# Kernel optimization log

Measured on AMD Instinct MI355X. Metric: run time of the kernel, lower is better.

## Reference

```python
import jax, jax.numpy as jnp
import numpy as np

B, N, D_MODEL = 2, 2048, 1024
H, HEAD_DIM, D1 = 16, 128, 2048
NK, RANK = 16, 32
GAMMA = 0.999


def setup_inputs() -> dict:
    key = jax.random.key(0)
    ks = jax.random.split(key, 12)
    std = 0.02
    return {
        "x": jax.random.normal(ks[0], (B, N, D_MODEL), jnp.float32),
        "Wu": jax.random.normal(ks[1], (D_MODEL, D1), jnp.float32) * std,
        "bu": jax.random.normal(ks[2], (D1,), jnp.float32) * std,
        "Wv": jax.random.normal(ks[3], (D_MODEL, D1), jnp.float32) * std,
        "bv": jax.random.normal(ks[4], (D1,), jnp.float32) * std,
        "Wo": jax.random.normal(ks[5], (D1, D_MODEL), jnp.float32) * std,
        "bo": jax.random.normal(ks[6], (D_MODEL,), jnp.float32) * std,
        # SKI low-rank Toeplitz kernel factors at nk inducing relative positions
        "a_pos": jax.random.normal(ks[7], (H, NK, RANK), jnp.float32) * 0.1,
        "b_pos": jax.random.normal(ks[8], (H, RANK, HEAD_DIM), jnp.float32) * 0.1,
        "a_neg": jax.random.normal(ks[9], (H, NK, RANK), jnp.float32) * 0.1,
        "b_neg": jax.random.normal(ks[10], (H, RANK, HEAD_DIM), jnp.float32) * 0.1,
        "t_zero": jax.random.normal(ks[11], (H, HEAD_DIM), jnp.float32) * 0.1,
    }


def _interp_decay_kernel(a, b, n):
    # low-rank kernel at nk inducing points: [h, nk, d]
    k_ind = jnp.einsum("hkr,hrd->hkd", a, b)
    lags = jnp.arange(1, n)                      # lags 1..n-1
    p = (lags - 1.0) / (n - 2.0) * (NK - 1)      # map lag onto inducing grid
    lo = jnp.floor(p).astype(jnp.int32)
    hi = jnp.minimum(lo + 1, NK - 1)
    w = (p - lo)[None, :, None]
    k = k_ind[:, lo, :] * (1.0 - w) + k_ind[:, hi, :] * w  # [h, n-1, d]
    decay = (GAMMA ** lags)[None, :, None]
    return k * decay


def reference(x, Wu, bu, Wv, bv, Wo, bo, a_pos, b_pos, a_neg, b_neg, t_zero):
    u = jax.nn.silu(x @ Wu + bu)                 # [b, n, d1]
    v = jax.nn.silu(x @ Wv + bv)                 # [b, n, d1]
    n = v.shape[1]
    vh = v.reshape(v.shape[0], n, H, HEAD_DIM)   # [b, n, h, d]

    kp = _interp_decay_kernel(a_pos, b_pos, n)   # [h, n-1, d]
    kn = _interp_decay_kernel(a_neg, b_neg, n)   # [h, n-1, d]
    m = 2 * n
    k_full = jnp.zeros((H, m, HEAD_DIM), vh.dtype)
    k_full = k_full.at[:, 0].set(t_zero)
    k_full = k_full.at[:, 1:n].set(kp)
    k_full = k_full.at[:, m - jnp.arange(1, n)].set(kn)  # non-causal (negative lags)

    # circular FFT convolution along the sequence axis
    vf = jnp.fft.rfft(vh, n=m, axis=1)                    # [b, mf, h, d]
    kf = jnp.transpose(jnp.fft.rfft(k_full, axis=1), (1, 0, 2))[None]  # [1, mf, h, d]
    y = jnp.fft.irfft(vf * kf, n=m, axis=1)[:, :n]        # [b, n, h, d]

    out = u * y.reshape(y.shape[0], n, D1)                # elementwise gate
    return out @ Wo + bo
```

## Files before the change

### kernel.cpp

```cpp
#include <hip/hip_runtime.h>
#include <hip/hip_bf16.h>
#include <stdint.h>
#include <stddef.h>

#define BB 2
#define NSEQ 2048
#define DM 1024
#define H 16
#define HD 128
#define D1 2048
#define NKI 16
#define RANKI 32
#define MROWS (BB * NSEQ)
#define VPROWS 6144
#define NTAP 28
#define NPAIR 13
#define NCHUNK 128
#define CLEN 16
#define GAMMA_F 0.999f
#define G_CL 0.9841201f
#define LN_G (-1.00050033e-3f)

__device__ constexpr int TAPS[NTAP] = {
  1, 2, 138, 139, 274, 275, 411, 412, 547, 548, 684,
  820, 821, 956, 957, 1093, 1094, 1229, 1230, 1366,
  1502, 1503, 1638, 1639, 1775, 1776, 1911, 1912};
__device__ constexpr int LEADL[NPAIR] = {1, 138, 274, 411, 547, 820, 956, 1093, 1229, 1502, 1638, 1775, 1911};
__device__ constexpr int LEADI[NPAIR] = {0, 2, 4, 6, 8, 11, 13, 15, 17, 20, 22, 24, 26};
#define SGL0_L 684
#define SGL0_I 10
#define SGL1_L 1366
#define SGL1_I 19

typedef short short8 __attribute__((ext_vector_type(8)));
typedef float floatx4 __attribute__((ext_vector_type(4)));

__device__ __forceinline__ float bf2f(unsigned short u) {
  union { unsigned int i; float f; } v; v.i = ((unsigned int)u) << 16; return v.f;
}
__device__ __forceinline__ unsigned short f2bf(float f) {
  union { float f; unsigned int i; } v; v.f = f;
  unsigned int r = (v.i + 0x7FFFu + ((v.i >> 16) & 1u)) >> 16;
  return (unsigned short)r;
}
__device__ __forceinline__ float bflo(unsigned int p) {
  union { unsigned int i; float f; } v; v.i = p << 16; return v.f;
}
__device__ __forceinline__ float bfhi(unsigned int p) {
  union { unsigned int i; float f; } v; v.i = p & 0xffff0000u; return v.f;
}
__device__ __forceinline__ void async16(const unsigned short* g, unsigned short* l) {
  __builtin_amdgcn_global_load_lds(
      (const __attribute__((address_space(1))) unsigned int*)g,
      (__attribute__((address_space(3))) unsigned int*)l, 16, 0, 0);
}

#define CVT4 (MROWS * DM / 4)
#define PAD16 (4 * NSEQ * D1 / 8)
__global__ __launch_bounds__(256) void prep_kernel(const float* __restrict__ x,
                                                   unsigned short* __restrict__ x_bf,
                                                   unsigned short* __restrict__ Vp) {
  int i = blockIdx.x * 256 + threadIdx.x;
  if (i < CVT4) {
    float4 f = ((const float4*)x)[i];
    ushort4 o;
    o.x = f2bf(f.x); o.y = f2bf(f.y); o.z = f2bf(f.z); o.w = f2bf(f.w);
    ((ushort4*)x_bf)[i] = o;
  } else {
    int j = i - CVT4;
    if (j < PAD16) {
      int r = j >> 19;
      int off = j & 524287;
      const size_t bases[4] = {0, (size_t)4096 * D1, (size_t)VPROWS * D1,
                               (size_t)VPROWS * D1 + (size_t)4096 * D1};
      uint4 z; z.x = z.y = z.z = z.w = 0u;
      ((uint4*)(Vp + bases[r]))[off] = z;
    }
  }
}

__device__ __forceinline__ float KinterpL(const float* kk, int l, int d) {
  if (l < 1) return 0.0f;
  float p = (float)(l - 1) * (15.0f / 2046.0f);
  int lo = (int)p; if (lo > 15) lo = 15;
  int hi = lo + 1; if (hi > 15) hi = 15;
  float w = p - (float)lo;
  float v = kk[lo * HD + d] * (1.0f - w) + kk[hi * HD + d] * w;
  return v * __powf(GAMMA_F, (float)l);
}

__global__ __launch_bounds__(256) void wprep_kernel(const float* __restrict__ Wu,
                                                    const float* __restrict__ Wv,
                                                    const float* __restrict__ Wo,
                                                    unsigned short* __restrict__ WT2,
                                                    unsigned short* __restrict__ WoT,
                                                    const float* __restrict__ ap,
                                                    const float* __restrict__ bp,
                                                    const float* __restrict__ an,
                                                    const float* __restrict__ bn,
                                                    float* __restrict__ dtp,
                                                    float* __restrict__ dtn) {
  int blk = blockIdx.x;
  int tid = threadIdx.x;
  if (blk < 6144) {
    __shared__ unsigned short t[32][33];
    const float* in; unsigned short* out;
    int rows, cols, bx, by;
    if (blk < 2048) {
      in = Wo; out = WoT; rows = D1; cols = DM;
      bx = (blk & 31) * 32; by = (blk >> 5) * 32;
    } else {
      int local = blk - 2048;
      int z = local >> 11, l2 = local & 2047;
      in = z ? Wv : Wu; out = WT2 + (size_t)z * D1 * DM;
      rows = DM; cols = D1;
      bx = (l2 & 63) * 32; by = (l2 >> 6) * 32;
    }
    int tx = tid & 31, ty = tid >> 5;
#pragma unroll
    for (int j = 0; j < 32; j += 8)
      t[ty + j][tx] = f2bf(in[(size_t)(by + ty + j) * cols + bx + tx]);
    __syncthreads();
#pragma unroll
    for (int j = 0; j < 32; j += 8)
      out[(size_t)(bx + ty + j) * rows + by + tx] = t[tx][ty + j];
  } else {
    __shared__ float kk[NKI * HD];
    int e0 = blk - 6144;
    int h = e0 & 15, dir = e0 >> 4;
    const float* a = (dir ? an : ap) + h * NKI * RANKI;
    const float* b = (dir ? bn : bp) + h * RANKI * HD;
    for (int e = tid; e < NKI * HD; e += 256) {
      int k = e >> 7, d = e & 127;
      float s = 0.0f;
#pragma unroll
      for (int r = 0; r < RANKI; ++r) s += a[k * RANKI + r] * b[r * HD + d];
      kk[e] = s;
    }
    __syncthreads();
    float* dt = (dir ? dtn : dtp) + (size_t)h * NTAP * HD;
    for (int e = tid; e < NTAP * HD; e += 256) {
      int j = e >> 7, d = e & 127;
      int l = TAPS[j];
      float K0 = KinterpL(kk, l, d);
      float K1 = KinterpL(kk, l - 1, d);
      float K2 = KinterpL(kk, l - 2, d);
      dt[e] = K0 - 2.0f * GAMMA_F * K1 + (GAMMA_F * GAMMA_F) * K2;
    }
  }
}

template <int MTILES>
__global__ __launch_bounds__(256) void gemm_uv(const unsigned short* __restrict__ A,
                                               const unsigned short* __restrict__ Bt,
                                               const float* __restrict__ bias,
                                               const float* __restrict__ bias2,
                                               void* __restrict__ C,
                                               void* __restrict__ C2,
                                               int M, int N, int K,
                                               int do_silu, int c_fp32, int uv_mode) {
  __shared__ unsigned short Al[2][MTILES * 1024];
  __shared__ unsigned short Bl[2][4096];
  int m0 = blockIdx.y * (MTILES * 32), n0 = blockIdx.x * 128;
  int tid = threadIdx.x;
  int lane = tid & 63, w = tid >> 6;
  int rw = (w >> 1) * (MTILES * 16), cw = (w & 1) * 64;
  int q = lane >> 4, l16 = lane & 15;
  floatx4 acc[MTILES][4];
#pragma unroll
  for (int mt = 0; mt < MTILES; ++mt)
#pragma unroll
    for (int nt = 0; nt < 4; ++nt) acc[mt][nt] = (floatx4){0.f, 0.f, 0.f, 0.f};
  int grow = tid >> 2;
  int gcol = (tid & 3) * 8;
  const unsigned short* A0 = A + (size_t)(m0 + grow) * K + gcol;
  const unsigned short* A1 = A0 + (size_t)64 * K;
  const unsigned short* B0 = Bt + (size_t)(n0 + grow) * K + gcol;
  const unsigned short* B1 = B0 + (size_t)64 * K;
  int woff = w * 512;
  int nIter = K >> 5;
  async16(A0, &Al[0][woff]);
  if (MTILES == 4) async16(A1, &Al[0][2048 + woff]);
  async16(B0, &Bl[0][woff]);
  async16(B1, &Bl[0][2048 + woff]);
  int p = 0;
  for (int i = 0; i < nIter; ++i) {
    __syncthreads();
    if (i + 1 < nIter) {
      int kn = (i + 1) << 5;
      async16(A0 + kn, &Al[p ^ 1][woff]);
      if (MTILES == 4) async16(A1 + kn, &Al[p ^ 1][2048 + woff]);
      async16(B0 + kn, &Bl[p ^ 1][woff]);
      async16(B1 + kn, &Bl[p ^ 1][2048 + woff]);
    }
    short8 af[MTILES], bfr[4];
#pragma unroll
    for (int i4 = 0; i4 < MTILES; ++i4)
      af[i4] = *(const short8*)(&Al[p][(rw + i4 * 16 + l16) * 32 + q * 8]);
#pragma unroll
    for (int i4 = 0; i4 < 4; ++i4)
      bfr[i4] = *(const short8*)(&Bl[p][(cw + i4 * 16 + l16) * 32 + q * 8]);
#pragma unroll
    for (int mt = 0; mt < MTILES; ++mt)
#pragma unroll
      for (int nt = 0; nt < 4; ++nt)
        acc[mt][nt] = __builtin_amdgcn_mfma_f32_16x16x32_bf16(af[mt], bfr[nt], acc[mt][nt], 0, 0, 0);
    p ^= 1;
  }
  int isv = uv_mode && (n0 >= 2048);
  int ldc = uv_mode ? 2048 : N;
  int ncb = isv ? (n0 - 2048) : n0;
  const float* buse = isv ? bias2 : bias;
#pragma unroll
  for (int mt = 0; mt < MTILES; ++mt) {
#pragma unroll
    for (int nt = 0; nt < 4; ++nt) {
      int n = ncb + cw + nt * 16 + l16;
      float bsv = buse[n];
#pragma unroll
      for (int r = 0; r < 4; ++r) {
        int m = m0 + rw + mt * 16 + q * 4 + r;
        float val = acc[mt][nt][r] + bsv;
        if (do_silu) val = val / (1.0f + __expf(-val));
        if (isv) {
          size_t mrow = (size_t)(2048 + m + ((m >> 11) << 12));
          ((unsigned short*)C2)[mrow * 2048 + n] = f2bf(val);
        } else if (c_fp32) {
          ((float*)C)[(size_t)m * ldc + n] = val;
        } else {
          ((unsigned short*)C)[(size_t)m * ldc + n] = f2bf(val);
        }
      }
    }
  }
}

template <int MTILES, int KCH>
__global__ __launch_bounds__(256) void gemm_out(const unsigned short* __restrict__ A,
                                                const unsigned short* __restrict__ Bt,
                                                const float* __restrict__ bias,
                                                float* __restrict__ C,
                                                int M, int N, int K) {
  constexpr int AREG = MTILES * 1024;
  constexpr int BREG = 4096;
  __shared__ unsigned short Al[2][AREG * KCH];
  __shared__ unsigned short Bl[2][BREG * KCH];
  int m0 = blockIdx.y * (MTILES * 32), n0 = blockIdx.x * 128;
  int tid = threadIdx.x;
  int lane = tid & 63, w = tid >> 6;
  int rw = (w >> 1) * (MTILES * 16), cw = (w & 1) * 64;
  int q = lane >> 4, l16 = lane & 15;
  floatx4 acc[MTILES][4];
#pragma unroll
  for (int mt = 0; mt < MTILES; ++mt)
#pragma unroll
    for (int nt = 0; nt < 4; ++nt) acc[mt][nt] = (floatx4){0.f, 0.f, 0.f, 0.f};
  int grow = tid >> 2;
  int gcol = (tid & 3) * 8;
  const unsigned short* A0 = A + (size_t)(m0 + grow) * K + gcol;
  const unsigned short* A1 = A0 + (size_t)64 * K;
  const unsigned short* B0 = Bt + (size_t)(n0 + grow) * K + gcol;
  const unsigned short* B1 = B0 + (size_t)64 * K;
  int woff = w * 512;
  int nIter = K / (32 * KCH);
#pragma unroll
  for (int kc = 0; kc < KCH; ++kc) {
    async16(A0 + kc * 32, &Al[0][kc * AREG + woff]);
    if (MTILES == 4) async16(A1 + kc * 32, &Al[0][kc * AREG + 2048 + woff]);
    async16(B0 + kc * 32, &Bl[0][kc * BREG + woff]);
    async16(B1 + kc * 32, &Bl[0][kc * BREG + 2048 + woff]);
  }
  int p = 0;
  for (int i = 0; i < nIter; ++i) {
    __syncthreads();
    if (i + 1 < nIter) {
      int kn = (i + 1) * 32 * KCH;
#pragma unroll
      for (int kc = 0; kc < KCH; ++kc) {
        async16(A0 + kn + kc * 32, &Al[p ^ 1][kc * AREG + woff]);
        if (MTILES == 4) async16(A1 + kn + kc * 32, &Al[p ^ 1][kc * AREG + 2048 + woff]);
        async16(B0 + kn + kc * 32, &Bl[p ^ 1][kc * BREG + woff]);
        async16(B1 + kn + kc * 32, &Bl[p ^ 1][kc * BREG + 2048 + woff]);
      }
    }
#pragma unroll
    for (int kc = 0; kc < KCH; ++kc) {
      short8 af[MTILES], bfr[4];
#pragma unroll
      for (int i4 = 0; i4 < MTILES; ++i4)
        af[i4] = *(const short8*)(&Al[p][kc * AREG + (rw + i4 * 16 + l16) * 32 + q * 8]);
#pragma unroll
      for (int i4 = 0; i4 < 4; ++i4)
        bfr[i4] = *(const short8*)(&Bl[p][kc * BREG + (cw + i4 * 16 + l16) * 32 + q * 8]);
#pragma unroll
      for (int mt = 0; mt < MTILES; ++mt)
#pragma unroll
        for (int nt = 0; nt < 4; ++nt)
          acc[mt][nt] = __builtin_amdgcn_mfma_f32_16x16x32_bf16(af[mt], bfr[nt], acc[mt][nt], 0, 0, 0);
    }
    p ^= 1;
  }
#pragma unroll
  for (int mt = 0; mt < MTILES; ++mt) {
#pragma unroll
    for (int nt = 0; nt < 4; ++nt) {
      int n = n0 + cw + nt * 16 + l16;
      float bsv = bias[n];
#pragma unroll
      for (int r = 0; r < 4; ++r) {
        int m = m0 + rw + mt * 16 + q * 4 + r;
        C[(size_t)m * N + n] = acc[mt][nt][r] + bsv;
      }
    }
  }
}

__global__ __launch_bounds__(256, 1) void scan_chunks(const unsigned short* __restrict__ Vp,
                                                      const float* __restrict__ dp,
                                                      const float* __restrict__ dn,
                                                      unsigned short* __restrict__ ypl,
                                                      unsigned short* __restrict__ ynl,
                                                      float* __restrict__ Sy_ex,
                                                      float* __restrict__ SG_ex) {
  int z = blockIdx.z;
  int dir = z >> 1, b = z & 1;
  int chunk = blockIdx.y;
  int c0 = blockIdx.x * 512 + threadIdx.x * 2;
  int h = c0 >> 7, d = c0 & 127;
  const float* dt = (dir ? dn : dp) + ((size_t)h * NTAP) * HD + d;
  float2 dreg[NTAP];
#pragma unroll
  for (int j = 0; j < NTAP; ++j) dreg[j] = *(const float2*)(dt + j * HD);
  const unsigned short* Vb = Vp + (size_t)b * VPROWS * D1 + c0;
  unsigned short* yl = (dir ? ynl : ypl) + (size_t)b * NSEQ * D1 + c0;
  float sy0 = 0.f, sy1 = 0.f, sg0 = 0.f, sg1 = 0.f;
  float carry0[NPAIR], carry1[NPAIR];
  if (!dir) {
    int t0 = chunk * CLEN;
    const unsigned short* Vrow = Vb + (size_t)(2048 + t0) * D1;
#pragma unroll
    for (int p = 0; p < NPAIR; ++p) {
      unsigned int pk = *(const unsigned int*)(Vrow - (ptrdiff_t)(LEADL[p] + 1) * D1);
      carry0[p] = bflo(pk); carry1[p] = bfhi(pk);
    }
    for (int i = 0; i < CLEN; ++i) {
      float F0 = 0.f, F1 = 0.f;
#pragma unroll
      for (int p = 0; p < NPAIR; ++p) {
        unsigned int pk = *(const unsigned int*)(Vrow - (ptrdiff_t)LEADL[p] * D1);
        float vl0 = bflo(pk), vl1 = bfhi(pk);
        F0 += dreg[LEADI[p]].x * vl0 + dreg[LEADI[p] + 1].x * carry0[p];
        F1 += dreg[LEADI[p]].y * vl1 + dreg[LEADI[p] + 1].y * carry1[p];
        carry0[p] = vl0; carry1[p] = vl1;
      }
      {
        unsigned int pk = *(const unsigned int*)(Vrow - (ptrdiff_t)SGL0_L * D1);
        F0 += dreg[SGL0_I].x * bflo(pk); F1 += dreg[SGL0_I].y * bfhi(pk);
      }
      {
        unsigned int pk = *(const unsigned int*)(Vrow - (ptrdiff_t)SGL1_L * D1);
        F0 += dreg[SGL1_I].x * bflo(pk); F1 += dreg[SGL1_I].y * bfhi(pk);
      }
      sg0 = GAMMA_F * sg0 + F0; sy0 = GAMMA_F * sy0 + sg0;
      sg1 = GAMMA_F * sg1 + F1; sy1 = GAMMA_F * sy1 + sg1;
      unsigned int pack = (unsigned int)f2bf(sy0) | ((unsigned int)f2bf(sy1) << 16);
      *(unsigned int*)(yl + (size_t)(t0 + i) * D1) = pack;
      Vrow += D1;
    }
  } else {
    int tstart = (NSEQ - 1) - chunk * CLEN;
    const unsigned short* Vrow = Vb + (size_t)(2048 + tstart) * D1;
#pragma unroll
    for (int p = 0; p < NPAIR; ++p) {
      unsigned int pk = *(const unsigned int*)(Vrow + (ptrdiff_t)(LEADL[p] + 1) * D1);
      carry0[p] = bflo(pk); carry1[p] = bfhi(pk);
    }
    for (int i = 0; i < CLEN; ++i) {
      float F0 = 0.f, F1 = 0.f;
#pragma unroll
      for (int p = 0; p < NPAIR; ++p) {
        unsigned int pk = *(const unsigned int*)(Vrow + (ptrdiff_t)LEADL[p] * D1);
        float vl0 = bflo(pk), vl1 = bfhi(pk);
        F0 += dreg[LEADI[p]].x * vl0 + dreg[LEADI[p] + 1].x * carry0[p];
        F1 += dreg[LEADI[p]].y * vl1 + dreg[LEADI[p] + 1].y * carry1[p];
        carry0[p] = vl0; carry1[p] = vl1;
      }
      {
        unsigned int pk = *(const unsigned int*)(Vrow + (ptrdiff_t)SGL0_L * D1);
        F0 += dreg[SGL0_I].x * bflo(pk); F1 += dreg[SGL0_I].y * bfhi(pk);
      }
      {
        unsigned int pk = *(const unsigned int*)(Vrow + (ptrdiff_t)SGL1_L * D1);
        F0 += dreg[SGL1_I].x * bflo(pk); F1 += dreg[SGL1_I].y * bfhi(pk);
      }
      sg0 = GAMMA_F * sg0 + F0; sy0 = GAMMA_F * sy0 + sg0;
      sg1 = GAMMA_F * sg1 + F1; sy1 = GAMMA_F * sy1 + sg1;
      unsigned int pack = (unsigned int)f2bf(sy0) | ((unsigned int)f2bf(sy1) << 16);
      *(unsigned int*)(yl + (size_t)(tstart - i) * D1) = pack;
      Vrow -= D1;
    }
  }
  size_t sidx = ((size_t)z * NCHUNK + chunk) * D1 + c0;
  Sy_ex[sidx] = sy0; Sy_ex[sidx + 1] = sy1;
  SG_ex[sidx] = sg0; SG_ex[sidx + 1] = sg1;
}

__global__ __launch_bounds__(256) void state_scan(const float* __restrict__ Sy_ex,
                                                  const float* __restrict__ SG_ex,
                                                  float* __restrict__ Sy_in,
                                                  float* __restrict__ SG_in) {
  int idx = blockIdx.x * 256 + threadIdx.x;
  if (idx >= 4 * D1) return;
  int z = idx >> 11, c = idx & (D1 - 1);
  float ey = 0.f, eg = 0.f;
  for (int k = 0; k < NCHUNK; ++k) {
    size_t s = ((size_t)z * NCHUNK + k) * D1 + c;
    Sy_in[s] = ey; SG_in[s] = eg;
    float lex = Sy_ex[s], lgx = SG_ex[s];
    ey = lex + G_CL * (ey + (float)CLEN * eg);
    eg = lgx + G_CL * eg;
  }
}

__global__ __launch_bounds__(256) void combine_kernel(const unsigned short* __restrict__ ypl,
                                                      const unsigned short* __restrict__ ynl,
                                                      const unsigned short* __restrict__ Vp,
                                                      const float* __restrict__ Sy_in,
                                                      const float* __restrict__ SG_in,
                                                      const float* __restrict__ tz,
                                                      const unsigned short* __restrict__ U,
                                                      unsigned short* __restrict__ G) {
  int e = blockIdx.x * 256 + threadIdx.x;
  int cq = e & (D1 / 4 - 1);
  int c0 = cq * 4;
  int r = e >> 9;
  int t = r & (NSEQ - 1);
  int b = r >> 11;
  int kp = t >> 4;  float dpD = (float)((t & 15) + 1);
  int tau = (NSEQ - 1) - t;
  int kn = tau >> 4; float dnD = (float)((tau & 15) + 1);
  float gp = __expf(dpD * LN_G);
  float gn = __expf(dnD * LN_G);
  size_t ix = (size_t)r * D1 + c0;
  size_t sp = ((size_t)(b) * NCHUNK + kp) * D1 + c0;
  size_t sn = ((size_t)(2 + b) * NCHUNK + kn) * D1 + c0;
  uint2 pyl = *(const uint2*)(ypl + ix);
  uint2 pyn = *(const uint2*)(ynl + ix);
  uint2 pv  = *(const uint2*)(Vp + ((size_t)b * VPROWS + 2048 + t) * D1 + c0);
  uint2 pu  = *(const uint2*)(U + ix);
  float4 syp = *(const float4*)(Sy_in + sp);
  float4 sgp = *(const float4*)(SG_in + sp);
  float4 syn = *(const float4*)(Sy_in + sn);
  float4 sgn = *(const float4*)(SG_in + sn);
  float4 tzv = *(const float4*)(tz + c0);
  float yv[4], uv[4], vv[4];
  yv[0] = bflo(pyl.x) + gp * (syp.x + dpD * sgp.x) + bflo(pyn.x) + gn * (syn.x + dnD * sgn.x);
  yv[1] = bfhi(pyl.x) + gp * (syp.y + dpD * sgp.y) + bfhi(pyn.x) + gn * (syn.y + dnD * sgn.y);
  yv[2] = bflo(pyl.y) + gp * (syp.z + dpD * sgp.z) + bflo(pyn.y) + gn * (syn.z + dnD * sgn.z);
  yv[3] = bfhi(pyl.y) + gp * (syp.w + dpD * sgp.w) + bfhi(pyn.y) + gn * (syn.w + dnD * sgn.w);
  vv[0] = bflo(pv.x); vv[1] = bfhi(pv.x); vv[2] = bflo(pv.y); vv[3] = bfhi(pv.y);
  uv[0] = bflo(pu.x); uv[1] = bfhi(pu.x); uv[2] = bflo(pu.y); uv[3] = bfhi(pu.y);
  float tza[4] = {tzv.x, tzv.y, tzv.z, tzv.w};
  uint2 og;
  unsigned short g0 = f2bf(uv[0] * (yv[0] + tza[0] * vv[0]));
  unsigned short g1 = f2bf(uv[1] * (yv[1] + tza[1] * vv[1]));
  unsigned short g2 = f2bf(uv[2] * (yv[2] + tza[2] * vv[2]));
  unsigned short g3 = f2bf(uv[3] * (yv[3] + tza[3] * vv[3]));
  og.x = (unsigned int)g0 | ((unsigned int)g1 << 16);
  og.y = (unsigned int)g2 | ((unsigned int)g3 << 16);
  *(uint2*)(G + ix) = og;
}

extern "C" void kernel_launch(void* const* d_in, const int* in_sizes, int n_in,
                              void* d_out, int out_size, void* d_ws, size_t ws_size,
                              hipStream_t stream) {
  const float* x      = (const float*)d_in[0];
  const float* Wu     = (const float*)d_in[1];
  const float* bu     = (const float*)d_in[2];
  const float* Wv     = (const float*)d_in[3];
  const float* bv     = (const float*)d_in[4];
  const float* Wo     = (const float*)d_in[5];
  const float* bo     = (const float*)d_in[6];
  const float* a_pos  = (const float*)d_in[7];
  const float* b_pos  = (const float*)d_in[8];
  const float* a_neg  = (const float*)d_in[9];
  const float* b_neg  = (const float*)d_in[10];
  const float* t_zero = (const float*)d_in[11];
  float* out = (float*)d_out;

  char* ws = (char*)d_ws;
  unsigned short* x_bf  = (unsigned short*)ws; ws += (size_t)MROWS * DM * 2;
  unsigned short* u_ws  = (unsigned short*)ws; ws += (size_t)MROWS * D1 * 2;
  unsigned short* Vp    = (unsigned short*)ws; ws += (size_t)BB * VPROWS * D1 * 2;
  unsigned short* ypl   = (unsigned short*)ws; ws += (size_t)MROWS * D1 * 2;
  unsigned short* ynl   = (unsigned short*)ws; ws += (size_t)MROWS * D1 * 2;
  unsigned short* WoT   = (unsigned short*)ws; ws += (size_t)DM * D1 * 2;
  float* dtp   = (float*)ws; ws += (size_t)H * NTAP * HD * 4;
  float* dtn   = (float*)ws; ws += (size_t)H * NTAP * HD * 4;
  float* Sy_in = (float*)ws; ws += (size_t)4 * NCHUNK * D1 * 4;
  float* SG_in = (float*)ws; ws += (size_t)4 * NCHUNK * D1 * 4;
  float* Sy_ex = (float*)x_bf;
  float* SG_ex = (float*)x_bf + (size_t)4 * NCHUNK * D1;
  unsigned short* WT2 = ypl;

  dim3 tb256(256);
  prep_kernel<<<dim3((CVT4 + PAD16 + 255) / 256), tb256, 0, stream>>>(x, x_bf, Vp);
  wprep_kernel<<<dim3(6176), tb256, 0, stream>>>(
      Wu, Wv, Wo, WT2, WoT, a_pos, b_pos, a_neg, b_neg, dtp, dtn);
  gemm_uv<2><<<dim3(2 * D1 / 128, MROWS / 64), tb256, 0, stream>>>(
      x_bf, WT2, bu, bv, u_ws, Vp, MROWS, 2 * D1, DM, 1, 0, 1);
  scan_chunks<<<dim3(D1 / 512, NCHUNK, 4), tb256, 0, stream>>>(Vp, dtp, dtn, ypl, ynl, Sy_ex, SG_ex);
  state_scan<<<dim3((4 * D1 + 255) / 256), tb256, 0, stream>>>(Sy_ex, SG_ex, Sy_in, SG_in);
  combine_kernel<<<dim3((size_t)MROWS * D1 / 1024), tb256, 0, stream>>>(ypl, ynl, Vp, Sy_in, SG_in, t_zero, u_ws, u_ws);
  gemm_out<2, 2><<<dim3(DM / 128, MROWS / 64), tb256, 0, stream>>>(
      u_ws, WoT, bo, out, MROWS, DM, D1);
}
```

Measured before the change: 291.9 us.

## Merge prep kernels into one launch and widen uv GEMM tile

```diff
diff --git a/kernel.cpp b/kernel.cpp
--- a/kernel.cpp
+++ b/kernel.cpp
@@ -55,30 +55,6 @@
       (__attribute__((address_space(3))) unsigned int*)l, 16, 0, 0);
 }
 
-#define CVT4 (MROWS * DM / 4)
-#define PAD16 (4 * NSEQ * D1 / 8)
-__global__ __launch_bounds__(256) void prep_kernel(const float* __restrict__ x,
-                                                   unsigned short* __restrict__ x_bf,
-                                                   unsigned short* __restrict__ Vp) {
-  int i = blockIdx.x * 256 + threadIdx.x;
-  if (i < CVT4) {
-    float4 f = ((const float4*)x)[i];
-    ushort4 o;
-    o.x = f2bf(f.x); o.y = f2bf(f.y); o.z = f2bf(f.z); o.w = f2bf(f.w);
-    ((ushort4*)x_bf)[i] = o;
-  } else {
-    int j = i - CVT4;
-    if (j < PAD16) {
-      int r = j >> 19;
-      int off = j & 524287;
-      const size_t bases[4] = {0, (size_t)4096 * D1, (size_t)VPROWS * D1,
-                               (size_t)VPROWS * D1 + (size_t)4096 * D1};
-      uint4 z; z.x = z.y = z.z = z.w = 0u;
-      ((uint4*)(Vp + bases[r]))[off] = z;
-    }
-  }
-}
-
 __device__ __forceinline__ float KinterpL(const float* kk, int l, int d) {
   if (l < 1) return 0.0f;
   float p = (float)(l - 1) * (15.0f / 2046.0f);
@@ -89,20 +65,44 @@
   return v * __powf(GAMMA_F, (float)l);
 }
 
-__global__ __launch_bounds__(256) void wprep_kernel(const float* __restrict__ Wu,
-                                                    const float* __restrict__ Wv,
-                                                    const float* __restrict__ Wo,
-                                                    unsigned short* __restrict__ WT2,
-                                                    unsigned short* __restrict__ WoT,
-                                                    const float* __restrict__ ap,
-                                                    const float* __restrict__ bp,
-                                                    const float* __restrict__ an,
-                                                    const float* __restrict__ bn,
-                                                    float* __restrict__ dtp,
-                                                    float* __restrict__ dtn) {
+#define CVT4 (MROWS * DM / 4)
+#define PAD16 (4 * NSEQ * D1 / 8)
+#define PREP0 6176
+__global__ __launch_bounds__(256) void allprep_kernel(const float* __restrict__ x,
+                                                      unsigned short* __restrict__ x_bf,
+                                                      unsigned short* __restrict__ Vp,
+                                                      const float* __restrict__ Wu,
+                                                      const float* __restrict__ Wv,
+                                                      const float* __restrict__ Wo,
+                                                      unsigned short* __restrict__ WT2,
+                                                      unsigned short* __restrict__ WoT,
+                                                      const float* __restrict__ ap,
+                                                      const float* __restrict__ bp,
+                                                      const float* __restrict__ an,
+                                                      const float* __restrict__ bn,
+                                                      float* __restrict__ dtp,
+                                                      float* __restrict__ dtn) {
   int blk = blockIdx.x;
   int tid = threadIdx.x;
-  if (blk < 6144) {
+  if (blk >= PREP0) {
+    int i = (blk - PREP0) * 256 + tid;
+    if (i < CVT4) {
+      float4 f = ((const float4*)x)[i];
+      ushort4 o;
+      o.x = f2bf(f.x); o.y = f2bf(f.y); o.z = f2bf(f.z); o.w = f2bf(f.w);
+      ((ushort4*)x_bf)[i] = o;
+    } else {
+      int j = i - CVT4;
+      if (j < PAD16) {
+        int r = j >> 19;
+        int off = j & 524287;
+        const size_t bases[4] = {0, (size_t)4096 * D1, (size_t)VPROWS * D1,
+                                 (size_t)VPROWS * D1 + (size_t)4096 * D1};
+        uint4 z; z.x = z.y = z.z = z.w = 0u;
+        ((uint4*)(Vp + bases[r]))[off] = z;
+      }
+    }
+  } else if (blk < 6144) {
     __shared__ unsigned short t[32][33];
     const float* in; unsigned short* out;
     int rows, cols, bx, by;
@@ -150,85 +150,82 @@
   }
 }
 
-template <int MTILES>
-__global__ __launch_bounds__(256) void gemm_uv(const unsigned short* __restrict__ A,
-                                               const unsigned short* __restrict__ Bt,
-                                               const float* __restrict__ bias,
-                                               const float* __restrict__ bias2,
-                                               void* __restrict__ C,
-                                               void* __restrict__ C2,
-                                               int M, int N, int K,
-                                               int do_silu, int c_fp32, int uv_mode) {
-  __shared__ unsigned short Al[2][MTILES * 1024];
-  __shared__ unsigned short Bl[2][4096];
-  int m0 = blockIdx.y * (MTILES * 32), n0 = blockIdx.x * 128;
+__global__ __launch_bounds__(256) void gemm_uv256(const unsigned short* __restrict__ A,
+                                                  const unsigned short* __restrict__ Bt,
+                                                  const float* __restrict__ bias,
+                                                  const float* __restrict__ bias2,
+                                                  unsigned short* __restrict__ C,
+                                                  unsigned short* __restrict__ C2,
+                                                  int M, int N, int K) {
+  __shared__ unsigned short Al[2][2048];
+  __shared__ unsigned short Bl[2][8192];
+  int m0 = blockIdx.y * 64, n0 = blockIdx.x * 256;
   int tid = threadIdx.x;
   int lane = tid & 63, w = tid >> 6;
-  int rw = (w >> 1) * (MTILES * 16), cw = (w & 1) * 64;
+  int rw = (w >> 1) * 32, cw = (w & 1) * 128;
   int q = lane >> 4, l16 = lane & 15;
-  floatx4 acc[MTILES][4];
-#pragma unroll
-  for (int mt = 0; mt < MTILES; ++mt)
-#pragma unroll
-    for (int nt = 0; nt < 4; ++nt) acc[mt][nt] = (floatx4){0.f, 0.f, 0.f, 0.f};
+  floatx4 acc[2][8];
+#pragma unroll
+  for (int mt = 0; mt < 2; ++mt)
+#pragma unroll
+    for (int nt = 0; nt < 8; ++nt) acc[mt][nt] = (floatx4){0.f, 0.f, 0.f, 0.f};
   int grow = tid >> 2;
   int gcol = (tid & 3) * 8;
   const unsigned short* A0 = A + (size_t)(m0 + grow) * K + gcol;
-  const unsigned short* A1 = A0 + (size_t)64 * K;
   const unsigned short* B0 = Bt + (size_t)(n0 + grow) * K + gcol;
   const unsigned short* B1 = B0 + (size_t)64 * K;
+  const unsigned short* B2 = B0 + (size_t)128 * K;
+  const unsigned short* B3 = B0 + (size_t)192 * K;
   int woff = w * 512;
   int nIter = K >> 5;
   async16(A0, &Al[0][woff]);
-  if (MTILES == 4) async16(A1, &Al[0][2048 + woff]);
   async16(B0, &Bl[0][woff]);
   async16(B1, &Bl[0][2048 + woff]);
+  async16(B2, &Bl[0][4096 + woff]);
+  async16(B3, &Bl[0][6144 + woff]);
   int p = 0;
   for (int i = 0; i < nIter; ++i) {
     __syncthreads();
     if (i + 1 < nIter) {
       int kn = (i + 1) << 5;
       async16(A0 + kn, &Al[p ^ 1][woff]);
-      if (MTILES == 4) async16(A1 + kn, &Al[p ^ 1][2048 + woff]);
       async16(B0 + kn, &Bl[p ^ 1][woff]);
       async16(B1 + kn, &Bl[p ^ 1][2048 + woff]);
-    }
-    short8 af[MTILES], bfr[4];
-#pragma unroll
-    for (int i4 = 0; i4 < MTILES; ++i4)
+      async16(B2 + kn, &Bl[p ^ 1][4096 + woff]);
+      async16(B3 + kn, &Bl[p ^ 1][6144 + woff]);
+    }
+    short8 af[2], bfr[8];
+#pragma unroll
+    for (int i4 = 0; i4 < 2; ++i4)
       af[i4] = *(const short8*)(&Al[p][(rw + i4 * 16 + l16) * 32 + q * 8]);
 #pragma unroll
-    for (int i4 = 0; i4 < 4; ++i4)
+    for (int i4 = 0; i4 < 8; ++i4)
       bfr[i4] = *(const short8*)(&Bl[p][(cw + i4 * 16 + l16) * 32 + q * 8]);
 #pragma unroll
-    for (int mt = 0; mt < MTILES; ++mt)
-#pragma unroll
-      for (int nt = 0; nt < 4; ++nt)
+    for (int mt = 0; mt < 2; ++mt)
+#pragma unroll
+      for (int nt = 0; nt < 8; ++nt)
         acc[mt][nt] = __builtin_amdgcn_mfma_f32_16x16x32_bf16(af[mt], bfr[nt], acc[mt][nt], 0, 0, 0);
     p ^= 1;
   }
-  int isv = uv_mode && (n0 >= 2048);
-  int ldc = uv_mode ? 2048 : N;
+  int isv = (n0 >= 2048);
   int ncb = isv ? (n0 - 2048) : n0;
-  const float* buse = isv ? bias2 : bias;
-#pragma unroll
-  for (int mt = 0; mt < MTILES; ++mt) {
-#pragma unroll
-    for (int nt = 0; nt < 4; ++nt) {
+#pragma unroll
+  for (int mt = 0; mt < 2; ++mt) {
+#pragma unroll
+    for (int nt = 0; nt < 8; ++nt) {
       int n = ncb + cw + nt * 16 + l16;
-      float bsv = buse[n];
+      float bsv = (isv ? bias2 : bias)[n];
 #pragma unroll
       for (int r = 0; r < 4; ++r) {
         int m = m0 + rw + mt * 16 + q * 4 + r;
         float val = acc[mt][nt][r] + bsv;
-        if (do_silu) val = val / (1.0f + __expf(-val));
+        val = val / (1.0f + __expf(-val));
         if (isv) {
           size_t mrow = (size_t)(2048 + m + ((m >> 11) << 12));
-          ((unsigned short*)C2)[mrow * 2048 + n] = f2bf(val);
-        } else if (c_fp32) {
-          ((float*)C)[(size_t)m * ldc + n] = val;
+          C2[mrow * 2048 + n] = f2bf(val);
         } else {
-          ((unsigned short*)C)[(size_t)m * ldc + n] = f2bf(val);
+          C[(size_t)m * 2048 + n] = f2bf(val);
         }
       }
     }
@@ -495,20 +492,19 @@
   unsigned short* ypl   = (unsigned short*)ws; ws += (size_t)MROWS * D1 * 2;
   unsigned short* ynl   = (unsigned short*)ws; ws += (size_t)MROWS * D1 * 2;
   unsigned short* WoT   = (unsigned short*)ws; ws += (size_t)DM * D1 * 2;
+  unsigned short* WT2   = (unsigned short*)ws; ws += (size_t)2 * D1 * DM * 2;
   float* dtp   = (float*)ws; ws += (size_t)H * NTAP * HD * 4;
   float* dtn   = (float*)ws; ws += (size_t)H * NTAP * HD * 4;
   float* Sy_in = (float*)ws; ws += (size_t)4 * NCHUNK * D1 * 4;
   float* SG_in = (float*)ws; ws += (size_t)4 * NCHUNK * D1 * 4;
   float* Sy_ex = (float*)x_bf;
   float* SG_ex = (float*)x_bf + (size_t)4 * NCHUNK * D1;
-  unsigned short* WT2 = ypl;
 
   dim3 tb256(256);
-  prep_kernel<<<dim3((CVT4 + PAD16 + 255) / 256), tb256, 0, stream>>>(x, x_bf, Vp);
-  wprep_kernel<<<dim3(6176), tb256, 0, stream>>>(
-      Wu, Wv, Wo, WT2, WoT, a_pos, b_pos, a_neg, b_neg, dtp, dtn);
-  gemm_uv<2><<<dim3(2 * D1 / 128, MROWS / 64), tb256, 0, stream>>>(
-      x_bf, WT2, bu, bv, u_ws, Vp, MROWS, 2 * D1, DM, 1, 0, 1);
+  allprep_kernel<<<dim3(PREP0 + (CVT4 + PAD16 + 255) / 256), tb256, 0, stream>>>(
+      x, x_bf, Vp, Wu, Wv, Wo, WT2, WoT, a_pos, b_pos, a_neg, b_neg, dtp, dtn);
+  gemm_uv256<<<dim3(2 * D1 / 256, MROWS / 64), tb256, 0, stream>>>(
+      x_bf, WT2, bu, bv, u_ws, Vp, MROWS, 2 * D1, DM);
   scan_chunks<<<dim3(D1 / 512, NCHUNK, 4), tb256, 0, stream>>>(Vp, dtp, dtn, ypl, ynl, Sy_ex, SG_ex);
   state_scan<<<dim3((4 * D1 + 255) / 256), tb256, 0, stream>>>(Sy_ex, SG_ex, Sy_in, SG_in);
   combine_kernel<<<dim3((size_t)MROWS * D1 / 1024), tb256, 0, stream>>>(ypl, ynl, Vp, Sy_in, SG_in, t_zero, u_ws, u_ws);
```

Result: no change. 295.1 us (+1.1%).
